# Optimization experiments

Hardware: AMD Instinct MI355X
Metric: run time of the kernel (lower is better)

The kernel has to match this reference:

```python
import jax, jax.numpy as jnp
import numpy as np
from jax import lax

KSIZE = 3
EPS_MASK = 1e-6
EPS_BN = 1e-5
DN = ('NCHW', 'OIHW', 'NCHW')
PAD = [(1, 1), (1, 1)]  # (k-1)*dilation//2 = 1 for k=3, d=1


def setup_inputs() -> dict:
    key = jax.random.key(0)
    kx, km, kw, kb = jax.random.split(key, 4)
    N, Cin, Cout, H, W_ = 8, 64, 128, 256, 256
    x = jax.random.normal(kx, (N, Cin, H, W_), dtype=jnp.float32)
    mask = (jax.random.uniform(km, (N, Cin, H, W_)) > 0.25).astype(jnp.float32)
    W = jax.random.normal(kw, (Cout, Cin, KSIZE, KSIZE), dtype=jnp.float32) * 0.05
    b = jax.random.normal(kb, (Cout,), dtype=jnp.float32) * 0.05
    gamma = jnp.ones((Cout,), dtype=jnp.float32)
    beta = jnp.zeros((Cout,), dtype=jnp.float32)
    return {"x": x, "mask": mask, "W": W, "b": b, "gamma": gamma, "beta": beta}


def reference(x, mask, W, b, gamma, beta):
    Cout, Cin = W.shape[0], W.shape[1]
    slide_winsize = float(Cin * KSIZE * KSIZE)

    # Mask-update conv: all-ones (Cout,Cin,k,k) kernel is identical across output
    # channels -> compute once with a single output channel and broadcast.
    ones_k = jnp.ones((1, Cin, KSIZE, KSIZE), dtype=mask.dtype)
    update = lax.conv_general_dilated(mask, ones_k, (1, 1), PAD,
                                      dimension_numbers=DN)  # [N,1,H,W]
    mask_ratio = slide_winsize / (update + EPS_MASK)
    update = jnp.clip(update, 0.0, 1.0)
    mask_ratio = mask_ratio * update

    # Dense conv on masked input
    raw = lax.conv_general_dilated(x * mask, W, (1, 1), PAD,
                                   dimension_numbers=DN)  # [N,Cout,H,W]
    bv = b[None, :, None, None]
    raw = raw + bv
    out = ((raw - bv) * mask_ratio + bv) * update

    # BatchNorm2d (training mode: batch statistics over N,H,W)
    mean = out.mean(axis=(0, 2, 3), keepdims=True)
    var = out.var(axis=(0, 2, 3), keepdims=True)
    out = (out - mean) * lax.rsqrt(var + EPS_BN)
    out = out * gamma[None, :, None, None] + beta[None, :, None, None]

    out = jax.nn.relu(out)
    update_full = jnp.broadcast_to(update, out.shape)  # matches torch [N,Cout,H,W]
    return out, update_full
```

## Files before the change

### kernel.cpp

```cpp
#include <hip/hip_runtime.h>

typedef __attribute__((ext_vector_type(8))) short bf16x8;
typedef __attribute__((ext_vector_type(8))) unsigned short u16x8;
typedef __attribute__((ext_vector_type(4))) float f32x4;
typedef unsigned int u32;

#define CI 64
#define CO 128
#define HH 256
#define WW 256
#define HP 258
#define WP 258
#define SLIDE 576.0f

__device__ __forceinline__ unsigned short f2bf(float f) {
  union { float f; unsigned int u; } c; c.f = f;
  unsigned int u = c.u;
  return (unsigned short)((u + 0x7FFFu + ((u >> 16) & 1u)) >> 16);
}
__device__ __forceinline__ float bf2f(unsigned short h) {
  union { unsigned int u; float f; } c; c.u = ((unsigned int)h) << 16;
  return c.f;
}

__global__ __launch_bounds__(256) void k_xm(const f32x4* __restrict__ x4,
                                            const f32x4* __restrict__ m4,
                                            unsigned short* __restrict__ xm,
                                            float4* __restrict__ msum4,
                                            const float* __restrict__ W,
                                            unsigned short* __restrict__ Wb) {
  __shared__ __align__(16) float tile[64 * 64 + 256];
  int b = blockIdx.x;
  int t = threadIdx.x;
  if (b >= 8192) {
    int blk = b - 8192;
    if (blk < 288) {
      int i = blk * 256 + t;
      int ci = i & 63, co = (i >> 6) & 127, tap = i >> 13;
      int kh = tap / 3, kw = tap - 3 * (tap / 3);
      Wb[i] = f2bf(W[((co * CI + ci) * 3 + kh) * 3 + kw]);
    } else {
      int i = (blk - 288) * 256 + t;
      if (i >= 8 * 1028) return;
      int n = i / 1028, p = i - n * 1028;
      int hh, wp;
      if (p < 258) { hh = 0; wp = p; }
      else if (p < 516) { hh = 257; wp = p - 258; }
      else { int q = p - 516; hh = 1 + (q >> 1); wp = (q & 1) * 257; }
      u16x8 z = {0, 0, 0, 0, 0, 0, 0, 0};
      unsigned short* d = xm + (((size_t)n * HP + hh) * WP + wp) * CI;
#pragma unroll
      for (int k = 0; k < 8; ++k) *(u16x8*)(d + k * 8) = z;
    }
    return;
  }
  int wt = b & 3, h = (b >> 2) & 255, n = b >> 10;
  int w0 = wt * 64;
  int p4 = t & 15, chg = t >> 4;
  size_t base = (size_t)n * CI * 16384 + (size_t)h * 64 + (w0 >> 2) + p4;
  float msx = 0.f, msy = 0.f, msz = 0.f, msw = 0.f;
#pragma unroll
  for (int j = 0; j < 4; ++j) {
    int ch = chg * 4 + j;
    size_t o = base + (size_t)ch * 16384;
    f32x4 xv = __builtin_nontemporal_load(&x4[o]);
    f32x4 mv = __builtin_nontemporal_load(&m4[o]);
    msx += mv.x; msy += mv.y; msz += mv.z; msw += mv.w;
    f32x4 pr = xv * mv;
    int kk = (ch >> 3) & 3;
    *(f32x4*)&tile[ch * 64 + ((p4 * 4) ^ (kk << 2))] = pr;
  }
  msx += __shfl_xor(msx, 16); msy += __shfl_xor(msy, 16);
  msz += __shfl_xor(msz, 16); msw += __shfl_xor(msw, 16);
  msx += __shfl_xor(msx, 32); msy += __shfl_xor(msy, 32);
  msz += __shfl_xor(msz, 32); msw += __shfl_xor(msw, 32);
  int wave = t >> 6, lane = t & 63;
  float4* red = (float4*)&tile[4096];
  if (lane < 16) red[wave * 16 + lane] = make_float4(msx, msy, msz, msw);
  __syncthreads();
  size_t dstb = (((size_t)n * HP + h + 1) * WP + (w0 + 1)) * CI;
#pragma unroll
  for (int iter = 0; iter < 2; ++iter) {
    int c = iter * 256 + t;
    int px = c >> 3, cg = c & 7;
    u16x8 v;
#pragma unroll
    for (int e = 0; e < 8; ++e) {
      int ch = cg * 8 + e;
      int kk = (ch >> 3) & 3;
      v[e] = f2bf(tile[ch * 64 + (px ^ (kk << 2))]);
    }
    *(u16x8*)(xm + dstb + (size_t)px * CI + cg * 8) = v;
  }
  if (t < 16) {
    float4 a = red[t], b2 = red[16 + t], c2 = red[32 + t], d2 = red[48 + t];
    float4 s;
    s.x = a.x + b2.x + c2.x + d2.x; s.y = a.y + b2.y + c2.y + d2.y;
    s.z = a.z + b2.z + c2.z + d2.z; s.w = a.w + b2.w + c2.w + d2.w;
    msum4[(size_t)n * 16384 + (size_t)h * 64 + (w0 >> 2) + t] = s;
  }
}

__global__ __launch_bounds__(256) void k_conv(
    const unsigned short* __restrict__ xm, const unsigned short* __restrict__ Wb,
    const float* __restrict__ msum, const float* __restrict__ bias,
    unsigned short* __restrict__ blob, float* __restrict__ psum, float* __restrict__ psq) {
  __shared__ __align__(16) char lds[51472];
  int b = blockIdx.x;
  int work = (b & 7) * 512 + (b >> 3);
  int wt = work & 1, h = (work >> 1) & 255, n = work >> 9;
  int w0 = wt * 128;
  int t = threadIdx.x;
  int lane = t & 63, wave = t >> 6;
  float* lr = (float*)(lds + 49920);
  float* lu = (float*)(lds + 50432);
  float* cs = (float*)(lds + 50944);
#pragma unroll
  for (int iter = 0; iter < 12; ++iter) {
    int c = iter * 256 + t;
    int r = (c >= 2080) ? 2 : (c >= 1040 ? 1 : 0);
    int cc = c - r * 1040;
    int wslot = cc >> 3, sub = cc & 7;
    int srcc = (wslot << 3) + (sub ^ (wslot & 7));
    const unsigned short* g = xm + (((size_t)n * HP + h + r) * WP + w0) * CI + (size_t)srcc * 8;
    u32 ldsoff = (u32)(r * 16640 + (((iter * 256 + (wave << 6)) - r * 1040) << 4));
    __builtin_amdgcn_global_load_lds((const __attribute__((address_space(1))) u32*)g,
        (__attribute__((address_space(3))) u32*)(void*)(lds + ldsoff), 16, 0, 0);
  }
  if (t < 48) {
    int c = 3072 + t;
    int cc = c - 2080;
    int wslot = cc >> 3, sub = cc & 7;
    int srcc = (wslot << 3) + (sub ^ (wslot & 7));
    const unsigned short* g = xm + (((size_t)n * HP + h + 2) * WP + w0) * CI + (size_t)srcc * 8;
    u32 ldsoff = (u32)(2 * 16640 + ((3072 - 2080) << 4));
    __builtin_amdgcn_global_load_lds((const __attribute__((address_space(1))) u32*)g,
        (__attribute__((address_space(3))) u32*)(void*)(lds + ldsoff), 16, 0, 0);
  }
  if (t < 130) {
    int w = w0 - 1 + t;
    float s = 0.f;
    if ((unsigned)w < 256u) {
      const float* mcol = msum + (size_t)n * 65536 + w;
      if (h >= 1) s += mcol[(h - 1) * 256];
      s += mcol[h * 256];
      if (h < 255) s += mcol[(h + 1) * 256];
    }
    cs[t] = s;
  }
  __syncthreads();
  if (t < 128) {
    float s = cs[t] + cs[t + 1] + cs[t + 2];
    float uc = fminf(s, 1.0f);
    lu[t] = uc;
    lr[t] = SLIDE / (s + 1e-6f) * uc;
  }

  int wm = wave >> 1, wn = wave & 1;
  int l15 = lane & 15, l4 = lane >> 4;
  f32x4 zero = {0.f, 0.f, 0.f, 0.f};
  f32x4 acc[4][4];
#pragma unroll
  for (int i = 0; i < 4; ++i)
#pragma unroll
    for (int j = 0; j < 4; ++j) acc[i][j] = zero;

#pragma unroll
  for (int kh = 0; kh < 3; ++kh) {
#pragma unroll
    for (int kw = 0; kw < 3; ++kw) {
      const unsigned short* wtap = Wb + ((kh * 3 + kw) * CO + wn * 64) * CI;
#pragma unroll
      for (int ks = 0; ks < 2; ++ks) {
        bf16x8 af[4], bfr[4];
#pragma unroll
        for (int mf = 0; mf < 4; ++mf) {
          int wslot = wm * 64 + mf * 16 + l15 + kw;
          int baddr = (((kh * 130 + wslot) << 7) + ks * 64 + l4 * 16) ^ ((wslot & 7) << 4);
          af[mf] = *(const bf16x8*)(lds + baddr);
        }
#pragma unroll
        for (int nf = 0; nf < 4; ++nf)
          bfr[nf] = *(const bf16x8*)(wtap + (nf * 16 + l15) * CI + ks * 32 + l4 * 8);
#pragma unroll
        for (int mf = 0; mf < 4; ++mf)
#pragma unroll
          for (int nf = 0; nf < 4; ++nf)
            acc[mf][nf] = __builtin_amdgcn_mfma_f32_16x16x32_bf16(af[mf], bfr[nf], acc[mf][nf], 0, 0, 0);
      }
    }
  }
  __syncthreads();

  float bv[4];
#pragma unroll
  for (int nf = 0; nf < 4; ++nf) bv[nf] = bias[wn * 64 + nf * 16 + l15];
  float rs_s[4] = {0.f, 0.f, 0.f, 0.f}, rq_s[4] = {0.f, 0.f, 0.f, 0.f};
  int px0 = wm * 64 + l4 * 4;
#pragma unroll
  for (int mf = 0; mf < 4; ++mf) {
    int pxb = px0 + mf * 16;
    float rs0 = lr[pxb], rs1 = lr[pxb + 1], rs2 = lr[pxb + 2], rs3 = lr[pxb + 3];
    float uc0 = lu[pxb], uc1 = lu[pxb + 1], uc2 = lu[pxb + 2], uc3 = lu[pxb + 3];
#pragma unroll
    for (int nf = 0; nf < 4; ++nf) {
      int co = wn * 64 + nf * 16 + l15;
      float v0 = acc[mf][nf][0] * rs0 + bv[nf] * uc0;
      float v1 = acc[mf][nf][1] * rs1 + bv[nf] * uc1;
      float v2 = acc[mf][nf][2] * rs2 + bv[nf] * uc2;
      float v3 = acc[mf][nf][3] * rs3 + bv[nf] * uc3;
      unsigned short h0 = f2bf(v0), h1 = f2bf(v1), h2 = f2bf(v2), h3 = f2bf(v3);
      float w0f = bf2f(h0), w1f = bf2f(h1), w2f = bf2f(h2), w3f = bf2f(h3);
      rs_s[nf] += w0f + w1f + w2f + w3f;
      rq_s[nf] += w0f * w0f + w1f * w1f + w2f * w2f + w3f * w3f;
      u32 lo = (u32)h0 | ((u32)h1 << 16);
      u32 hi = (u32)h2 | ((u32)h3 << 16);
      *(uint2*)(lds + co * 272 + pxb * 2) = make_uint2(lo, hi);
    }
  }
  float* sred = (float*)(lds + 34816);
#pragma unroll
  for (int nf = 0; nf < 4; ++nf) {
    float s = rs_s[nf], q = rq_s[nf];
    s += __shfl_xor(s, 16); s += __shfl_xor(s, 32);
    q += __shfl_xor(q, 16); q += __shfl_xor(q, 32);
    if (l4 == 0) {
      sred[(wave * 4 + nf) * 16 + l15] = s;
      sred[256 + (wave * 4 + nf) * 16 + l15] = q;
    }
  }
  __syncthreads();
  int pixrow = (n * CO) << 16;
#pragma unroll
  for (int iter = 0; iter < 8; ++iter) {
    int i = iter * 256 + t;
    int co = i >> 4, oct = i & 15;
    u16x8 v = *(const u16x8*)(lds + co * 272 + oct * 16);
    *(u16x8*)(blob + (size_t)(pixrow + (co << 16) + (h << 8) + w0 + oct * 8)) = v;
  }
  int co = t & 127;
  int wn2 = co >> 6, nf2 = (co >> 4) & 3, cc2 = co & 15;
  float a0 = sred[(wn2 * 4 + nf2) * 16 + cc2] + sred[((2 + wn2) * 4 + nf2) * 16 + cc2];
  float a1 = sred[256 + (wn2 * 4 + nf2) * 16 + cc2] + sred[256 + ((2 + wn2) * 4 + nf2) * 16 + cc2];
  if (t < 128) psum[(size_t)b * 128 + co] = a0;
  else         psq[(size_t)b * 128 + co]  = a1;
}

__global__ void k_bnstats(const float* __restrict__ psum, const float* __restrict__ psq,
                          const float* __restrict__ gamma, const float* __restrict__ beta,
                          float* __restrict__ bn_scale, float* __restrict__ bn_shift) {
  int co = blockIdx.x;
  int t = threadIdx.x;
  float s = 0.f, q = 0.f;
  for (int i = t; i < 4096; i += 256) {
    s += psum[(size_t)i * 128 + co];
    q += psq[(size_t)i * 128 + co];
  }
#pragma unroll
  for (int o = 1; o < 64; o <<= 1) { s += __shfl_xor(s, o); q += __shfl_xor(q, o); }
  __shared__ float red[8];
  int wv = t >> 6, ln = t & 63;
  if (ln == 0) { red[wv] = s; red[4 + wv] = q; }
  __syncthreads();
  if (t == 0) {
    s = red[0] + red[1] + red[2] + red[3];
    q = red[4] + red[5] + red[6] + red[7];
    const float inv = 1.0f / 524288.0f;
    float mean = s * inv;
    float var = q * inv - mean * mean;
    float sc = gamma[co] * rsqrtf(var + 1e-5f);
    bn_scale[co] = sc;
    bn_shift[co] = beta[co] - mean * sc;
  }
}

__global__ __launch_bounds__(256) void k_out(const unsigned short* __restrict__ blob,
                                             const float* __restrict__ msum,
                                             const float* __restrict__ bn_scale,
                                             const float* __restrict__ bn_shift,
                                             float* __restrict__ out,
                                             float* __restrict__ upd) {
  __shared__ float lu[256];
  __shared__ float cs[258];
  int b = blockIdx.x;
  int h = b & 255, n = b >> 8;
  int t = threadIdx.x;
  if (t < 258) {
    int w = t - 1;
    float s = 0.f;
    if ((unsigned)w < 256u) {
      const float* mcol = msum + (size_t)n * 65536 + w;
      if (h >= 1) s += mcol[(h - 1) * 256];
      s += mcol[h * 256];
      if (h < 255) s += mcol[(h + 1) * 256];
    }
    cs[t] = s;
  }
  __syncthreads();
  if (t < 256) lu[t] = fminf(cs[t] + cs[t + 1] + cs[t + 2], 1.0f);
  __syncthreads();
  size_t rowbase = ((size_t)(n * CO) << 16) + (h << 8);
#pragma unroll
  for (int iter = 0; iter < 32; ++iter) {
    int i = iter * 256 + t;
    int c = i >> 6, q = i & 63;
    size_t off = rowbase + ((size_t)c << 16) + q * 4;
    uint2 raw = *(const uint2*)(blob + off);
    float sc = bn_scale[c], sh = bn_shift[c];
    f32x4 v;
    v.x = fmaxf(bf2f((unsigned short)(raw.x & 0xFFFF)) * sc + sh, 0.f);
    v.y = fmaxf(bf2f((unsigned short)(raw.x >> 16)) * sc + sh, 0.f);
    v.z = fmaxf(bf2f((unsigned short)(raw.y & 0xFFFF)) * sc + sh, 0.f);
    v.w = fmaxf(bf2f((unsigned short)(raw.y >> 16)) * sc + sh, 0.f);
    __builtin_nontemporal_store(v, (f32x4*)(out + off));
    f32x4 uv = *(const f32x4*)&lu[q * 4];
    __builtin_nontemporal_store(uv, (f32x4*)(upd + off));
  }
}

extern "C" void kernel_launch(void* const* d_in, const int* in_sizes, int n_in,
                              void* d_out, int out_size, void* d_ws, size_t ws_size,
                              hipStream_t stream) {
  (void)in_sizes; (void)n_in; (void)out_size; (void)ws_size;
  const float* x     = (const float*)d_in[0];
  const float* mask  = (const float*)d_in[1];
  const float* W     = (const float*)d_in[2];
  const float* bias  = (const float*)d_in[3];
  const float* gamma = (const float*)d_in[4];
  const float* beta  = (const float*)d_in[5];

  float* out = (float*)d_out;
  float* upd_out = out + 67108864;

  char* wsb = (char*)d_ws;
  unsigned short* Wb = (unsigned short*)wsb;
  float* msum     = (float*)(wsb + (2u << 20));
  float* bn_scale = (float*)(wsb + (8u << 20));
  float* bn_shift = bn_scale + 128;
  float* part_sum = (float*)(wsb + (9u << 20));
  float* part_sq  = (float*)(wsb + (11u << 20));
  unsigned short* xm   = (unsigned short*)(wsb + (16u << 20));
  unsigned short* blob = (unsigned short*)(wsb + (96u << 20));

  k_xm<<<8513, 256, 0, stream>>>((const f32x4*)x, (const f32x4*)mask, xm,
                                 (float4*)msum, W, Wb);
  k_conv<<<4096, 256, 0, stream>>>(xm, Wb, msum, bias, blob, part_sum, part_sq);
  k_bnstats<<<128, 256, 0, stream>>>(part_sum, part_sq, gamma, beta, bn_scale, bn_shift);
  k_out<<<2048, 256, 0, stream>>>(blob, msum, bn_scale, bn_shift, out, upd_out);
}
```

Before: 343.6 us.

## Retile conv blocks to 2 rows x 64 px and widen output kernel loads

```diff
diff --git a/kernel.cpp b/kernel.cpp
--- a/kernel.cpp
+++ b/kernel.cpp
@@ -105,58 +105,65 @@
     const unsigned short* __restrict__ xm, const unsigned short* __restrict__ Wb,
     const float* __restrict__ msum, const float* __restrict__ bias,
     unsigned short* __restrict__ blob, float* __restrict__ psum, float* __restrict__ psq) {
-  __shared__ __align__(16) char lds[51472];
+  __shared__ __align__(16) char lds[38432];
   int b = blockIdx.x;
   int work = (b & 7) * 512 + (b >> 3);
-  int wt = work & 1, h = (work >> 1) & 255, n = work >> 9;
-  int w0 = wt * 128;
+  int wt = work & 3, h2 = (work >> 2) & 127, n = work >> 9;
+  int hb = h2 * 2;
+  int w0 = wt * 64;
   int t = threadIdx.x;
   int lane = t & 63, wave = t >> 6;
-  float* lr = (float*)(lds + 49920);
-  float* lu = (float*)(lds + 50432);
-  float* cs = (float*)(lds + 50944);
-#pragma unroll
-  for (int iter = 0; iter < 12; ++iter) {
+  float* sred = (float*)(lds + 34816);
+  float* lr   = (float*)(lds + 36864);
+  float* lu   = (float*)(lds + 37376);
+  float* cs0  = (float*)(lds + 37888);
+  float* cs1  = (float*)(lds + 38160);
+#pragma unroll
+  for (int iter = 0; iter < 8; ++iter) {
     int c = iter * 256 + t;
-    int r = (c >= 2080) ? 2 : (c >= 1040 ? 1 : 0);
-    int cc = c - r * 1040;
+    int r = (c >= 1584) ? 3 : (c >= 1056) ? 2 : (c >= 528) ? 1 : 0;
+    int cc = c - r * 528;
     int wslot = cc >> 3, sub = cc & 7;
     int srcc = (wslot << 3) + (sub ^ (wslot & 7));
-    const unsigned short* g = xm + (((size_t)n * HP + h + r) * WP + w0) * CI + (size_t)srcc * 8;
-    u32 ldsoff = (u32)(r * 16640 + (((iter * 256 + (wave << 6)) - r * 1040) << 4));
+    const unsigned short* g = xm + (((size_t)n * HP + hb + r) * WP + w0) * CI + (size_t)srcc * 8;
+    u32 ldsoff = (u32)((iter * 256 + (wave << 6)) << 4);
     __builtin_amdgcn_global_load_lds((const __attribute__((address_space(1))) u32*)g,
         (__attribute__((address_space(3))) u32*)(void*)(lds + ldsoff), 16, 0, 0);
   }
-  if (t < 48) {
-    int c = 3072 + t;
-    int cc = c - 2080;
+  if (t < 64) {
+    int c = 2048 + t;
+    int cc = c - 1584;
     int wslot = cc >> 3, sub = cc & 7;
     int srcc = (wslot << 3) + (sub ^ (wslot & 7));
-    const unsigned short* g = xm + (((size_t)n * HP + h + 2) * WP + w0) * CI + (size_t)srcc * 8;
-    u32 ldsoff = (u32)(2 * 16640 + ((3072 - 2080) << 4));
+    const unsigned short* g = xm + (((size_t)n * HP + hb + 3) * WP + w0) * CI + (size_t)srcc * 8;
+    u32 ldsoff = (u32)(2048 << 4);
     __builtin_amdgcn_global_load_lds((const __attribute__((address_space(1))) u32*)g,
         (__attribute__((address_space(3))) u32*)(void*)(lds + ldsoff), 16, 0, 0);
   }
-  if (t < 130) {
+  if (t < 66) {
     int w = w0 - 1 + t;
-    float s = 0.f;
+    float m0 = 0.f, m1 = 0.f, m2 = 0.f, m3 = 0.f;
     if ((unsigned)w < 256u) {
       const float* mcol = msum + (size_t)n * 65536 + w;
-      if (h >= 1) s += mcol[(h - 1) * 256];
-      s += mcol[h * 256];
-      if (h < 255) s += mcol[(h + 1) * 256];
-    }
-    cs[t] = s;
+      if (hb >= 1) m0 = mcol[(hb - 1) * 256];
+      m1 = mcol[hb * 256];
+      m2 = mcol[(hb + 1) * 256];
+      if (hb + 2 < 256) m3 = mcol[(hb + 2) * 256];
+    }
+    cs0[t] = m0 + m1 + m2;
+    cs1[t] = m1 + m2 + m3;
   }
   __syncthreads();
   if (t < 128) {
-    float s = cs[t] + cs[t + 1] + cs[t + 2];
+    int row = t >> 6, px = t & 63;
+    const float* csr = row ? cs1 : cs0;
+    float s = csr[px] + csr[px + 1] + csr[px + 2];
     float uc = fminf(s, 1.0f);
     lu[t] = uc;
     lr[t] = SLIDE / (s + 1e-6f) * uc;
   }
 
-  int wm = wave >> 1, wn = wave & 1;
+  int wrow = wave >> 1, wn = wave & 1;
   int l15 = lane & 15, l4 = lane >> 4;
   f32x4 zero = {0.f, 0.f, 0.f, 0.f};
   f32x4 acc[4][4];
@@ -167,6 +174,7 @@
 
 #pragma unroll
   for (int kh = 0; kh < 3; ++kh) {
+    int rr = wrow + kh;
 #pragma unroll
     for (int kw = 0; kw < 3; ++kw) {
       const unsigned short* wtap = Wb + ((kh * 3 + kw) * CO + wn * 64) * CI;
@@ -175,8 +183,8 @@
         bf16x8 af[4], bfr[4];
 #pragma unroll
         for (int mf = 0; mf < 4; ++mf) {
-          int wslot = wm * 64 + mf * 16 + l15 + kw;
-          int baddr = (((kh * 130 + wslot) << 7) + ks * 64 + l4 * 16) ^ ((wslot & 7) << 4);
+          int ws = mf * 16 + l15 + kw;
+          int baddr = (((rr * 66 + ws) << 7) + ks * 64 + l4 * 16) ^ ((ws & 7) << 4);
           af[mf] = *(const bf16x8*)(lds + baddr);
         }
 #pragma unroll
@@ -196,12 +204,12 @@
 #pragma unroll
   for (int nf = 0; nf < 4; ++nf) bv[nf] = bias[wn * 64 + nf * 16 + l15];
   float rs_s[4] = {0.f, 0.f, 0.f, 0.f}, rq_s[4] = {0.f, 0.f, 0.f, 0.f};
-  int px0 = wm * 64 + l4 * 4;
+  int pxr = wrow << 6;
 #pragma unroll
   for (int mf = 0; mf < 4; ++mf) {
-    int pxb = px0 + mf * 16;
-    float rs0 = lr[pxb], rs1 = lr[pxb + 1], rs2 = lr[pxb + 2], rs3 = lr[pxb + 3];
-    float uc0 = lu[pxb], uc1 = lu[pxb + 1], uc2 = lu[pxb + 2], uc3 = lu[pxb + 3];
+    int pxb = mf * 16 + l4 * 4;
+    float rs0 = lr[pxr + pxb], rs1 = lr[pxr + pxb + 1], rs2 = lr[pxr + pxb + 2], rs3 = lr[pxr + pxb + 3];
+    float uc0 = lu[pxr + pxb], uc1 = lu[pxr + pxb + 1], uc2 = lu[pxr + pxb + 2], uc3 = lu[pxr + pxb + 3];
 #pragma unroll
     for (int nf = 0; nf < 4; ++nf) {
       int co = wn * 64 + nf * 16 + l15;
@@ -215,10 +223,9 @@
       rq_s[nf] += w0f * w0f + w1f * w1f + w2f * w2f + w3f * w3f;
       u32 lo = (u32)h0 | ((u32)h1 << 16);
       u32 hi = (u32)h2 | ((u32)h3 << 16);
-      *(uint2*)(lds + co * 272 + pxb * 2) = make_uint2(lo, hi);
-    }
-  }
-  float* sred = (float*)(lds + 34816);
+      *(uint2*)(lds + co * 272 + (wrow << 7) + pxb * 2) = make_uint2(lo, hi);
+    }
+  }
 #pragma unroll
   for (int nf = 0; nf < 4; ++nf) {
     float s = rs_s[nf], q = rq_s[nf];
@@ -230,13 +237,12 @@
     }
   }
   __syncthreads();
-  int pixrow = (n * CO) << 16;
 #pragma unroll
   for (int iter = 0; iter < 8; ++iter) {
     int i = iter * 256 + t;
-    int co = i >> 4, oct = i & 15;
-    u16x8 v = *(const u16x8*)(lds + co * 272 + oct * 16);
-    *(u16x8*)(blob + (size_t)(pixrow + (co << 16) + (h << 8) + w0 + oct * 8)) = v;
+    int co = i >> 4, rr2 = (i >> 3) & 1, oct = i & 7;
+    u16x8 v = *(const u16x8*)(lds + co * 272 + rr2 * 128 + oct * 16);
+    *(u16x8*)(blob + ((size_t)(n * CO + co) << 16) + ((hb + rr2) << 8) + w0 + oct * 8) = v;
   }
   int co = t & 127;
   int wn2 = co >> 6, nf2 = (co >> 4) & 3, cc2 = co & 15;
@@ -282,6 +288,7 @@
                                              float* __restrict__ upd) {
   __shared__ float lu[256];
   __shared__ float cs[258];
+  __shared__ float lsc[128], lsh[128];
   int b = blockIdx.x;
   int h = b & 255, n = b >> 8;
   int t = threadIdx.x;
@@ -296,25 +303,33 @@
     }
     cs[t] = s;
   }
+  if (t < 128) { lsc[t] = bn_scale[t]; lsh[t] = bn_shift[t]; }
   __syncthreads();
   if (t < 256) lu[t] = fminf(cs[t] + cs[t + 1] + cs[t + 2], 1.0f);
   __syncthreads();
   size_t rowbase = ((size_t)(n * CO) << 16) + (h << 8);
 #pragma unroll
-  for (int iter = 0; iter < 32; ++iter) {
+  for (int iter = 0; iter < 16; ++iter) {
     int i = iter * 256 + t;
-    int c = i >> 6, q = i & 63;
-    size_t off = rowbase + ((size_t)c << 16) + q * 4;
-    uint2 raw = *(const uint2*)(blob + off);
-    float sc = bn_scale[c], sh = bn_shift[c];
-    f32x4 v;
-    v.x = fmaxf(bf2f((unsigned short)(raw.x & 0xFFFF)) * sc + sh, 0.f);
-    v.y = fmaxf(bf2f((unsigned short)(raw.x >> 16)) * sc + sh, 0.f);
-    v.z = fmaxf(bf2f((unsigned short)(raw.y & 0xFFFF)) * sc + sh, 0.f);
-    v.w = fmaxf(bf2f((unsigned short)(raw.y >> 16)) * sc + sh, 0.f);
-    __builtin_nontemporal_store(v, (f32x4*)(out + off));
-    f32x4 uv = *(const f32x4*)&lu[q * 4];
-    __builtin_nontemporal_store(uv, (f32x4*)(upd + off));
+    int c = i >> 5, q8 = i & 31;
+    size_t off = rowbase + ((size_t)c << 16) + q8 * 8;
+    u16x8 raw = *(const u16x8*)(blob + off);
+    float sc = lsc[c], sh = lsh[c];
+    f32x4 v0, v1;
+    v0.x = fmaxf(bf2f((unsigned short)raw[0]) * sc + sh, 0.f);
+    v0.y = fmaxf(bf2f((unsigned short)raw[1]) * sc + sh, 0.f);
+    v0.z = fmaxf(bf2f((unsigned short)raw[2]) * sc + sh, 0.f);
+    v0.w = fmaxf(bf2f((unsigned short)raw[3]) * sc + sh, 0.f);
+    v1.x = fmaxf(bf2f((unsigned short)raw[4]) * sc + sh, 0.f);
+    v1.y = fmaxf(bf2f((unsigned short)raw[5]) * sc + sh, 0.f);
+    v1.z = fmaxf(bf2f((unsigned short)raw[6]) * sc + sh, 0.f);
+    v1.w = fmaxf(bf2f((unsigned short)raw[7]) * sc + sh, 0.f);
+    __builtin_nontemporal_store(v0, (f32x4*)(out + off));
+    __builtin_nontemporal_store(v1, (f32x4*)(out + off + 4));
+    f32x4 u0 = *(const f32x4*)&lu[q8 * 8];
+    f32x4 u1 = *(const f32x4*)&lu[q8 * 8 + 4];
+    __builtin_nontemporal_store(u0, (f32x4*)(upd + off));
+    __builtin_nontemporal_store(u1, (f32x4*)(upd + off + 4));
   }
 }
 
```

Result: slower. 455.2 us (+32.5%).
